# Kernel tuning notes

Measured on AMD Instinct MI355X. Metric: run time of the kernel, lower is better.

Reference implementation:

```python
import jax, jax.numpy as jnp
import numpy as np

DIM_HEAD = 128
HEADS = 16
SCALE = DIM_HEAD ** -0.5


def rotate_half(t):
    # '... (j d) -> ... j d' with j=2: split into first/second halves
    x1, x2 = jnp.split(t, 2, axis=-1)
    return jnp.concatenate((-x2, x1), axis=-1)


def apply_rope(pos, t):
    # pos: [n, d]; t: [..., n, d]
    return t * jnp.cos(pos) + rotate_half(t) * jnp.sin(pos)


def setup_inputs() -> dict:
    key = jax.random.key(0)
    k0, k1, k2, k3 = jax.random.split(key, 4)
    b, n, dim = 2, 2048, 2048
    inner = HEADS * DIM_HEAD
    return {
        "x": jax.random.normal(k0, (b, n, dim), jnp.float32),
        "Wq": jax.random.normal(k1, (dim, inner), jnp.float32) * 0.02,
        "Wkv": jax.random.normal(k2, (dim, 2 * DIM_HEAD), jnp.float32) * 0.02,
        "Wout": jax.random.normal(k3, (inner, dim), jnp.float32) * 0.02,
    }


def reference(x, Wq, Wkv, Wout):
    b, n, dim = x.shape
    # projections from the UN-normalized x (norm in original is dead code)
    q = x @ Wq                               # [b, n, h*d]
    kv = x @ Wkv                             # [b, n, 2d]
    k, v = jnp.split(kv, 2, axis=-1)         # each [b, n, d] (multi-query)
    q = q.reshape(b, n, HEADS, DIM_HEAD).transpose(0, 2, 1, 3)  # [b,h,n,d]

    # rotary positions
    inv_freq = 1.0 / (10000.0 ** (jnp.arange(0, DIM_HEAD, 2, dtype=jnp.float32) / DIM_HEAD))
    freqs = jnp.arange(n, dtype=jnp.float32)[:, None] * inv_freq[None, :]
    pos = jnp.concatenate((freqs, freqs), axis=-1)  # [n, d]

    q = apply_rope(pos, q) * SCALE
    k = apply_rope(pos, k)

    sim = jnp.einsum('bhid,bjd->bhij', q, k)  # [b,h,n,n]
    causal_mask = jnp.triu(jnp.ones((n, n), dtype=bool), 1)
    neg = -jnp.finfo(sim.dtype).max
    sim = jnp.where(causal_mask, neg, sim)
    sim = sim - jax.lax.stop_gradient(jnp.max(sim, axis=-1, keepdims=True))
    attn = jax.nn.softmax(sim, axis=-1)

    out = jnp.einsum('bhij,bjd->bhid', attn, v)          # [b,h,n,d]
    out = out.transpose(0, 2, 1, 3).reshape(b, n, HEADS * DIM_HEAD)
    return out @ Wout
```

## Files before the change

kernel.cpp:

```cpp
#include <hip/hip_runtime.h>
#include <hip/hip_bf16.h>
#include <cstddef>
#include <cstdint>

#define BATCH 2
#define SEQ   2048
#define DIM   2048
#define HEADS 16
#define DHEAD 128
#define INNER (HEADS * DHEAD)
#define MROWS (BATCH * SEQ)
#define ATT_SCALE 0.08838834764831845f
#define QK_SCALE (0.08838834764831845f * 1.4426950408889634f)
#define NEG_LOG2_10000_DIV64 (-13.287712379549449f / 64.0f)
#define M_HAT 12.0f

typedef __attribute__((ext_vector_type(8))) short short8;
typedef __attribute__((ext_vector_type(4))) short short4v;
typedef __attribute__((ext_vector_type(4))) float f32x4;

static __device__ __forceinline__ short f2bf(float x) {
    uint32_t u = __float_as_uint(x);
    uint32_t r = (u + 0x7fffu + ((u >> 16) & 1u)) >> 16;
    return (short)r;
}
static __device__ __forceinline__ float bf2f(short s) {
    return __uint_as_float(((uint32_t)(uint16_t)s) << 16);
}
static __device__ __forceinline__ short2 f2bf2(float a, float b) {
    __hip_bfloat162 h = __float22bfloat162_rn(make_float2(a, b));
    return *reinterpret_cast<short2*>(&h);
}

static __device__ __forceinline__ void glds16(const short* g, short* l) {
    __builtin_amdgcn_global_load_lds(
        (const __attribute__((address_space(1))) unsigned int*)g,
        (__attribute__((address_space(3))) unsigned int*)l, 16, 0, 0);
}

static __device__ __forceinline__ int swz_row(int r) {
    return (r & 3) | ((r >> 1) & 4);
}

static __device__ __forceinline__ void tcast_body(const float* __restrict__ W,
                                                  short* __restrict__ Wt,
                                                  int R, int C, int bx, int by,
                                                  int tid, float (*tile)[65]) {
    const int c0 = bx * 64, r0 = by * 64;
#pragma unroll
    for (int t = 0; t < 16; ++t) {
        int idx = tid + t * 256;
        int row = idx >> 6, col = idx & 63;
        tile[row][col] = W[(size_t)(r0 + row) * C + c0 + col];
    }
    __syncthreads();
#pragma unroll
    for (int t = 0; t < 16; ++t) {
        int idx = tid + t * 256;
        int r = idx >> 6, c = idx & 63;
        Wt[(size_t)(c0 + r) * R + r0 + c] = f2bf(tile[c][r]);
    }
}

__global__ __launch_bounds__(256) void prep(const float* __restrict__ x,
                                            short* __restrict__ xb,
                                            const float* __restrict__ Wq,
                                            short* __restrict__ Wt,
                                            const float* __restrict__ Wkv,
                                            short* __restrict__ Wkvt,
                                            const float* __restrict__ Wout,
                                            short* __restrict__ WtO,
                                            float2* __restrict__ lut) {
    __shared__ float tile[64][65];
    const int bid = blockIdx.x;
    const int tid = threadIdx.x;
    if (bid < 8192) {
        int i = bid * 256 + tid;
        float4 v = ((const float4*)x)[i];
        short2 s01 = f2bf2(v.x, v.y), s23 = f2bf2(v.z, v.w);
        short4v s = {s01.x, s01.y, s23.x, s23.y};
        ((short4v*)xb)[i] = s;
    } else if (bid < 9216) {
        int t = bid - 8192;
        tcast_body(Wq, Wt, DIM, INNER, t & 31, t >> 5, tid, tile);
    } else if (bid < 9344) {
        int t = bid - 9216;
        tcast_body(Wkv, Wkvt, DIM, 256, t & 3, t >> 2, tid, tile);
    } else if (bid < 10368) {
        int t = bid - 9344;
        tcast_body(Wout, WtO, INNER, DIM, t & 31, t >> 5, tid, tile);
    } else {
        int t = (bid - 10368) * 256 + tid;
        int pos = t >> 6, j = t & 63;
        float ang = (float)pos * exp2f((float)j * NEG_LOG2_10000_DIV64);
        lut[t] = make_float2(cosf(ang), sinf(ang));
    }
}

__global__ __launch_bounds__(256) void gemm_qkv(const short* __restrict__ A,
                                                const short* __restrict__ Bt,
                                                short* __restrict__ qout,
                                                short* __restrict__ kvout) {
    __shared__ __align__(16) short sA[128 * 32];
    __shared__ __align__(16) short sB[128 * 32];
    const int K = DIM;

    const int tid = threadIdx.x;
    const int w = tid >> 6, lane = tid & 63;
    const int ln = lane & 15, qr = lane >> 4;
    const int bm = blockIdx.y * 128, bn = blockIdx.x * 128;
    const int wm = (w >> 1) * 64, wn = (w & 1) * 64;

    const f32x4 zero4 = {0.f, 0.f, 0.f, 0.f};
    f32x4 acc[4][4];
#pragma unroll
    for (int mt = 0; mt < 4; ++mt)
#pragma unroll
        for (int nt = 0; nt < 4; ++nt) acc[mt][nt] = zero4;

    const int srow = lane >> 2;
    const short* pA = A + (size_t)(bm + w * 32 + srow) * K + (lane & 3) * 8;
    const short* pB = Bt + (size_t)(bn + w * 32 + srow) * K + (lane & 3) * 8;
    short* lA = &sA[(w * 32) * 32];
    short* lB = &sB[(w * 32) * 32];

    for (int k0 = 0; k0 < K; k0 += 32) {
        __syncthreads();
        glds16(pA + k0, lA);
        glds16(pA + k0 + (size_t)16 * K, lA + 512);
        glds16(pB + k0, lB);
        glds16(pB + k0 + (size_t)16 * K, lB + 512);
        __syncthreads();

        short8 af[4], bfr[4];
#pragma unroll
        for (int mt = 0; mt < 4; ++mt)
            af[mt] = *(const short8*)&sA[(wm + mt * 16 + ln) * 32 + qr * 8];
#pragma unroll
        for (int nt = 0; nt < 4; ++nt)
            bfr[nt] = *(const short8*)&sB[(wn + nt * 16 + ln) * 32 + qr * 8];
#pragma unroll
        for (int mt = 0; mt < 4; ++mt)
#pragma unroll
            for (int nt = 0; nt < 4; ++nt)
                acc[mt][nt] = __builtin_amdgcn_mfma_f32_16x16x32_bf16(
                    af[mt], bfr[nt], acc[mt][nt], 0, 0, 0);
    }

    short* C;
    int stride, colb;
    if (bn < INNER) { C = qout; stride = INNER; colb = bn; }
    else            { C = kvout; stride = 256;  colb = bn - INNER; }
#pragma unroll
    for (int mt = 0; mt < 4; ++mt)
#pragma unroll
        for (int nt = 0; nt < 4; ++nt)
#pragma unroll
            for (int r = 0; r < 4; ++r)
                C[(size_t)(bm + wm + mt * 16 + qr * 4 + r) * stride +
                  colb + wn + nt * 16 + ln] = f2bf(acc[mt][nt][r]);
}

__global__ __launch_bounds__(256) void gemm_bt(const short* __restrict__ A,
                                               const short* __restrict__ Bt,
                                               float* __restrict__ C,
                                               int M, int N, int K) {
    __shared__ __align__(16) short sA[128 * 32];
    __shared__ __align__(16) short sB[128 * 32];

    const int tid = threadIdx.x;
    const int w = tid >> 6, lane = tid & 63;
    const int ln = lane & 15, qr = lane >> 4;
    const int bm = blockIdx.y * 128, bn = blockIdx.x * 128;
    const int wm = (w >> 1) * 64, wn = (w & 1) * 64;

    const f32x4 zero4 = {0.f, 0.f, 0.f, 0.f};
    f32x4 acc[4][4];
#pragma unroll
    for (int mt = 0; mt < 4; ++mt)
#pragma unroll
        for (int nt = 0; nt < 4; ++nt) acc[mt][nt] = zero4;

    const int srow = lane >> 2;
    const short* pA = A + (size_t)(bm + w * 32 + srow) * K + (lane & 3) * 8;
    const short* pB = Bt + (size_t)(bn + w * 32 + srow) * K + (lane & 3) * 8;
    short* lA = &sA[(w * 32) * 32];
    short* lB = &sB[(w * 32) * 32];

    for (int k0 = 0; k0 < K; k0 += 32) {
        __syncthreads();
        glds16(pA + k0, lA);
        glds16(pA + k0 + (size_t)16 * K, lA + 512);
        glds16(pB + k0, lB);
        glds16(pB + k0 + (size_t)16 * K, lB + 512);
        __syncthreads();

        short8 af[4], bfr[4];
#pragma unroll
        for (int mt = 0; mt < 4; ++mt)
            af[mt] = *(const short8*)&sA[(wm + mt * 16 + ln) * 32 + qr * 8];
#pragma unroll
        for (int nt = 0; nt < 4; ++nt)
            bfr[nt] = *(const short8*)&sB[(wn + nt * 16 + ln) * 32 + qr * 8];
#pragma unroll
        for (int mt = 0; mt < 4; ++mt)
#pragma unroll
            for (int nt = 0; nt < 4; ++nt)
                acc[mt][nt] = __builtin_amdgcn_mfma_f32_16x16x32_bf16(
                    af[mt], bfr[nt], acc[mt][nt], 0, 0, 0);
    }

#pragma unroll
    for (int mt = 0; mt < 4; ++mt)
#pragma unroll
        for (int nt = 0; nt < 4; ++nt)
#pragma unroll
            for (int r = 0; r < 4; ++r)
                C[(size_t)(bm + wm + mt * 16 + qr * 4 + r) * N +
                  bn + wn + nt * 16 + ln] = acc[mt][nt][r];
}

__global__ __launch_bounds__(256) void rope_q_v(short* __restrict__ qb,
                                                const float2* __restrict__ lut) {
    int idx = blockIdx.x * 256 + threadIdx.x;
    int c = idx & 7;
    int rh = idx >> 3;
    int pos = (rh >> 4) & (SEQ - 1);
    short* row = qb + ((size_t)rh << 7);
    short8 a8 = *(short8*)&row[c * 8];
    short8 b8 = *(short8*)&row[64 + c * 8];
    const float2* lp = &lut[pos * 64 + c * 8];
    short8 o1, o2;
#pragma unroll
    for (int e = 0; e < 8; e += 2) {
        float2 cs0 = lp[e], cs1 = lp[e + 1];
        float a0 = bf2f(a8[e]), b0 = bf2f(b8[e]);
        float a1 = bf2f(a8[e + 1]), b1 = bf2f(b8[e + 1]);
        short2 p1 = f2bf2((a0 * cs0.x - b0 * cs0.y) * QK_SCALE,
                          (a1 * cs1.x - b1 * cs1.y) * QK_SCALE);
        short2 p2 = f2bf2((b0 * cs0.x + a0 * cs0.y) * QK_SCALE,
                          (b1 * cs1.x + a1 * cs1.y) * QK_SCALE);
        o1[e] = p1.x; o1[e + 1] = p1.y;
        o2[e] = p2.x; o2[e + 1] = p2.y;
    }
    *(short8*)&row[c * 8] = o1;
    *(short8*)&row[64 + c * 8] = o2;
}

__global__ __launch_bounds__(256) void prep_kv(const short* __restrict__ kvbb,
                                               short* __restrict__ kb,
                                               short* __restrict__ vt,
                                               const float2* __restrict__ lut) {
    __shared__ float tile[64][65];
    const int bid = blockIdx.x;
    const int tid = threadIdx.x;
    if (bid < 128) {
        const int b = bid >> 6;
        const int tile_id = bid & 63;
        const int p0 = (tile_id >> 1) * 64;
        const int d0 = (tile_id & 1) * 64;
#pragma unroll
        for (int t = 0; t < 16; ++t) {
            int idx = tid + t * 256;
            int row = idx >> 6, col = idx & 63;
            tile[row][col] = bf2f(kvbb[((size_t)(b * SEQ) + p0 + row) * 256 + 128 + d0 + col]);
        }
        __syncthreads();
#pragma unroll
        for (int t = 0; t < 16; ++t) {
            int idx = tid + t * 256;
            int r = idx >> 6, c = idx & 63;
            vt[((size_t)(b * DHEAD) + d0 + r) * SEQ + p0 + c] = f2bf(tile[c][r]);
        }
    } else {
        int t = (bid - 128) * 256 + tid;
        int c = t & 7;
        int bn = t >> 3;
        int pos = bn & (SEQ - 1);
        const short* row = kvbb + (size_t)bn * 256;
        short* orow = kb + ((size_t)bn << 7);
        short8 a8 = *(const short8*)&row[c * 8];
        short8 b8 = *(const short8*)&row[64 + c * 8];
        const float2* lp = &lut[pos * 64 + c * 8];
        short8 o1, o2;
#pragma unroll
        for (int e = 0; e < 8; e += 2) {
            float2 cs0 = lp[e], cs1 = lp[e + 1];
            float a0 = bf2f(a8[e]), b0 = bf2f(b8[e]);
            float a1 = bf2f(a8[e + 1]), b1 = bf2f(b8[e + 1]);
            short2 p1 = f2bf2(a0 * cs0.x - b0 * cs0.y, a1 * cs1.x - b1 * cs1.y);
            short2 p2 = f2bf2(b0 * cs0.x + a0 * cs0.y, b1 * cs1.x + a1 * cs1.y);
            o1[e] = p1.x; o1[e + 1] = p1.y;
            o2[e] = p2.x; o2[e + 1] = p2.y;
        }
        *(short8*)&orow[c * 8] = o1;
        *(short8*)&orow[64 + c * 8] = o2;
    }
}

__global__ __launch_bounds__(512) void attn_mfma(const short* __restrict__ qb,
                                                 const short* __restrict__ kb,
                                                 const short* __restrict__ vt,
                                                 short* __restrict__ o) {
    __shared__ __align__(16) short sK[2][2][64 * 128];
    __shared__ __align__(16) short sV[2][2][128 * 64];
    __shared__ float lred[4][2][64];

    const int bid = blockIdx.x;
    const int p = bid & 7;
    const int bh = bid >> 3;
    const int h = bh & (HEADS - 1);
    const int b = bh >> 4;

    const int tid = threadIdx.x;
    const int w = tid >> 6;
    const int g = w >> 2;
    const int wg = w & 3;
    const int lane = tid & 63;
    const int ln = lane & 15;
    const int qr = lane >> 4;

    const short* kbase = kb + (size_t)b * SEQ * DHEAD;
    const short* vbase = vt + (size_t)b * DHEAD * SEQ;

    int offK[4], offV[4], ldsK[4], ldsV[4];
#pragma unroll
    for (int t = 0; t < 4; ++t) {
        int rk = wg * 16 + t * 4 + (lane >> 4);
        int ck = (lane & 15) ^ swz_row(rk);
        offK[t] = rk * DHEAD + ck * 8;
        ldsK[t] = (wg * 16 + t * 4) * 128;
        int rv = wg * 32 + t * 8 + (lane >> 3);
        int cv = (lane & 7) ^ swz_row(rv);
        offV[t] = rv * SEQ + cv * 8;
        ldsV[t] = (wg * 32 + t * 8) * 64;
    }

    for (int ph = 0; ph < 2; ++ph) {
        const int it = ph ? p : (15 - p);
        const int i0 = it * 128;
        const int njt = 2 * it + 2;
        const int half = njt >> 1;
        const int igmax = i0 + wg * 32 + 31;

        short8 qf[2][4];
#pragma unroll
        for (int qs = 0; qs < 2; ++qs) {
            const size_t qrow =
                ((size_t)(b * SEQ + i0 + wg * 32 + qs * 16 + ln)) * INNER + h * DHEAD;
#pragma unroll
            for (int ks = 0; ks < 4; ++ks)
                qf[qs][ks] = *(const short8*)&qb[qrow + ks * 32 + qr * 8];
        }

        const f32x4 zero4 = {0.f, 0.f, 0.f, 0.f};
        const f32x4 mhat4 = {-M_HAT, -M_HAT, -M_HAT, -M_HAT};
        f32x4 oa[2][8];
#pragma unroll
        for (int qs = 0; qs < 2; ++qs)
#pragma unroll
            for (int dt = 0; dt < 8; ++dt) oa[qs][dt] = zero4;
        float lsum[2] = {0.f, 0.f};

        __syncthreads();
        {
            const size_t kof = (size_t)g * 64 * DHEAD;
            const size_t vof = (size_t)g * 64;
#pragma unroll
            for (int t = 0; t < 4; ++t)
                glds16(kbase + kof + offK[t], &sK[g][0][ldsK[t]]);
#pragma unroll
            for (int t = 0; t < 4; ++t)
                glds16(vbase + vof + offV[t], &sV[g][0][ldsV[t]]);
        }

        for (int k = 0; k < half; ++k) {
            const int cur = k & 1;
            const int jt = 2 * k + g;
            __syncthreads();
            if (k + 1 < half) {
                const size_t kof = (size_t)(jt + 2) * 64 * DHEAD;
                const size_t vof = (size_t)(jt + 2) * 64;
#pragma unroll
                for (int t = 0; t < 4; ++t)
                    glds16(kbase + kof + offK[t], &sK[g][cur ^ 1][ldsK[t]]);
#pragma unroll
                for (int t = 0; t < 4; ++t)
                    glds16(vbase + vof + offV[t], &sV[g][cur ^ 1][ldsV[t]]);
            }
            if (jt * 64 > igmax) continue;

            f32x4 sacc[2][4];
#pragma unroll
            for (int qs = 0; qs < 2; ++qs)
#pragma unroll
                for (int nt = 0; nt < 4; ++nt) sacc[qs][nt] = mhat4;
            __builtin_amdgcn_s_setprio(1);
#pragma unroll
            for (int nt = 0; nt < 4; ++nt) {
                const int row = ((nt >> 1) << 5) + ((ln >> 2) << 3) +
                                ((nt & 1) << 2) + (ln & 3);
                const int sw = ln & 7;
#pragma unroll
                for (int ks = 0; ks < 4; ++ks) {
                    short8 kf = *(const short8*)&sK[g][cur][row * 128 + ((4 * ks + qr) ^ sw) * 8];
                    sacc[0][nt] = __builtin_amdgcn_mfma_f32_16x16x32_bf16(
                        kf, qf[0][ks], sacc[0][nt], 0, 0, 0);
                    sacc[1][nt] = __builtin_amdgcn_mfma_f32_16x16x32_bf16(
                        kf, qf[1][ks], sacc[1][nt], 0, 0, 0);
                }
            }
            __builtin_amdgcn_s_setprio(0);

            short8 pb[2][2];
#pragma unroll
            for (int qs = 0; qs < 2; ++qs) {
                const int ig = i0 + wg * 32 + qs * 16 + ln;
                if (jt * 64 + 63 > ig) {
#pragma unroll
                    for (int nt = 0; nt < 4; ++nt)
#pragma unroll
                        for (int r = 0; r < 4; ++r) {
                            int jg = jt * 64 + ((nt >> 1) << 5) + qr * 8 +
                                     ((nt & 1) << 2) + r;
                            if (jg > ig) sacc[qs][nt][r] = -3.0e38f;
                        }
                }
                float rs = 0.f;
                float pv[4][4];
#pragma unroll
                for (int nt = 0; nt < 4; ++nt)
#pragma unroll
                    for (int r = 0; r < 4; ++r) {
                        float e = exp2f(sacc[qs][nt][r]);
                        pv[nt][r] = e;
                        rs += e;
                    }
                rs += __shfl_xor(rs, 16);
                rs += __shfl_xor(rs, 32);
                lsum[qs] += rs;
#pragma unroll
                for (int kb2 = 0; kb2 < 2; ++kb2) {
                    short2* pp = (short2*)&pb[qs][kb2];
                    pp[0] = f2bf2(pv[2 * kb2][0], pv[2 * kb2][1]);
                    pp[1] = f2bf2(pv[2 * kb2][2], pv[2 * kb2][3]);
                    pp[2] = f2bf2(pv[2 * kb2 + 1][0], pv[2 * kb2 + 1][1]);
                    pp[3] = f2bf2(pv[2 * kb2 + 1][2], pv[2 * kb2 + 1][3]);
                }
            }

            __builtin_amdgcn_s_setprio(1);
#pragma unroll
            for (int kb2 = 0; kb2 < 2; ++kb2) {
#pragma unroll
                for (int dt = 0; dt < 8; ++dt) {
                    const int row = dt * 16 + ln;
                    short8 vf = *(const short8*)&sV[g][cur][row * 64 +
                        ((4 * kb2 + qr) ^ swz_row(row)) * 8];
                    oa[0][dt] = __builtin_amdgcn_mfma_f32_16x16x32_bf16(
                        vf, pb[0][kb2], oa[0][dt], 0, 0, 0);
                    oa[1][dt] = __builtin_amdgcn_mfma_f32_16x16x32_bf16(
                        vf, pb[1][kb2], oa[1][dt], 0, 0, 0);
                }
            }
            __builtin_amdgcn_s_setprio(0);
        }

        f32x4* cb = (f32x4*)&sK[1][0][0];
        __syncthreads();
        if (g == 1) {
#pragma unroll
            for (int dt = 0; dt < 8; ++dt)
                cb[dt * 256 + wg * 64 + lane] = oa[0][dt];
            lred[wg][0][lane] = lsum[0];
            lred[wg][1][lane] = lsum[1];
        }
        __syncthreads();
        if (g == 0) {
#pragma unroll
            for (int dt = 0; dt < 8; ++dt)
                oa[0][dt] += cb[dt * 256 + wg * 64 + lane];
            lsum[0] += lred[wg][0][lane];
            lsum[1] += lred[wg][1][lane];
        }
        __syncthreads();
        if (g == 1) {
#pragma unroll
            for (int dt = 0; dt < 8; ++dt)
                cb[dt * 256 + wg * 64 + lane] = oa[1][dt];
        }
        __syncthreads();
        if (g == 0) {
#pragma unroll
            for (int dt = 0; dt < 8; ++dt)
                oa[1][dt] += cb[dt * 256 + wg * 64 + lane];
#pragma unroll
            for (int qs = 0; qs < 2; ++qs) {
                const float invl = 1.f / lsum[qs];
                short* orow = o + ((size_t)(b * SEQ + i0 + wg * 32 + qs * 16 + ln)) * INNER +
                              h * DHEAD;
#pragma unroll
                for (int dt = 0; dt < 8; ++dt) {
                    short2 s01 = f2bf2(oa[qs][dt][0] * invl, oa[qs][dt][1] * invl);
                    short2 s23 = f2bf2(oa[qs][dt][2] * invl, oa[qs][dt][3] * invl);
                    short4v sv = {s01.x, s01.y, s23.x, s23.y};
                    *(short4v*)&orow[dt * 16 + qr * 4] = sv;
                }
            }
        }
    }
}

extern "C" void kernel_launch(void* const* d_in, const int* in_sizes, int n_in,
                              void* d_out, int out_size, void* d_ws, size_t ws_size,
                              hipStream_t stream) {
    const float* x    = (const float*)d_in[0];
    const float* Wq   = (const float*)d_in[1];
    const float* Wkv  = (const float*)d_in[2];
    const float* Wout = (const float*)d_in[3];
    float* out = (float*)d_out;

    short* xb    = (short*)d_ws;
    short* Wt    = xb + (size_t)MROWS * DIM;
    short* Wkvt  = Wt + (size_t)DIM * INNER;
    short* WtO   = Wkvt + (size_t)256 * DIM;
    short* qb    = WtO + (size_t)DIM * INNER;
    short* kvbb  = qb + (size_t)MROWS * INNER;
    short* kb    = kvbb + (size_t)MROWS * 256;
    short* vt    = kb + (size_t)MROWS * DHEAD;
    float2* lut  = (float2*)(vt + (size_t)BATCH * DHEAD * SEQ);
    short* ob    = xb;

    prep<<<10880, 256, 0, stream>>>(x, xb, Wq, Wt, Wkv, Wkvt, Wout, WtO, lut);
    gemm_qkv<<<dim3(18, 32), 256, 0, stream>>>(xb, Wt, qb, kvbb);
    rope_q_v<<<(MROWS * HEADS * 8) / 256, 256, 0, stream>>>(qb, lut);
    prep_kv<<<256, 256, 0, stream>>>(kvbb, kb, vt, lut);
    attn_mfma<<<256, 512, 0, stream>>>(qb, kb, vt, ob);
    gemm_bt<<<dim3(DIM / 128, MROWS / 128), 256, 0, stream>>>(ob, WtO, out, MROWS, DIM, INNER);
}
```

Measured before the change: 290.7 us.

## Fuse RoPE into QKV GEMM epilogue, remap GEMM blocks per XCD, vectorize transposes

RoPE for Q (with the softmax scale) and for K is now applied in the QKV GEMM epilogue. Each block stages its accumulator tile in LDS so it can read the partner half-dimension. This removes the separate rope_q_v kernel and the K-rope half of prep_kv, along with their extra global read/write passes. Both GEMMs also remap block IDs round-robin across the 8 XCDs for better L2 locality, and the weight transpose-cast uses float4 loads and short4 stores. The cost is a larger LDS footprint and an extra sync in the QKV epilogue, plus more scattered per-element stores there.

```diff
diff --git a/kernel.cpp b/kernel.cpp
--- a/kernel.cpp
+++ b/kernel.cpp
@@ -48,17 +48,24 @@
                                                   int tid, float (*tile)[65]) {
     const int c0 = bx * 64, r0 = by * 64;
 #pragma unroll
-    for (int t = 0; t < 16; ++t) {
+    for (int t = 0; t < 4; ++t) {
         int idx = tid + t * 256;
-        int row = idx >> 6, col = idx & 63;
-        tile[row][col] = W[(size_t)(r0 + row) * C + c0 + col];
+        int row = idx >> 4, col4 = idx & 15;
+        float4 v = *(const float4*)&W[(size_t)(r0 + row) * C + c0 + col4 * 4];
+        tile[row][col4 * 4 + 0] = v.x;
+        tile[row][col4 * 4 + 1] = v.y;
+        tile[row][col4 * 4 + 2] = v.z;
+        tile[row][col4 * 4 + 3] = v.w;
     }
     __syncthreads();
 #pragma unroll
-    for (int t = 0; t < 16; ++t) {
+    for (int t = 0; t < 4; ++t) {
         int idx = tid + t * 256;
-        int r = idx >> 6, c = idx & 63;
-        Wt[(size_t)(c0 + r) * R + r0 + c] = f2bf(tile[c][r]);
+        int r = idx >> 4, c4 = idx & 15;
+        short2 s01 = f2bf2(tile[c4 * 4 + 0][r], tile[c4 * 4 + 1][r]);
+        short2 s23 = f2bf2(tile[c4 * 4 + 2][r], tile[c4 * 4 + 3][r]);
+        short4v s = {s01.x, s01.y, s23.x, s23.y};
+        *(short4v*)&Wt[(size_t)(c0 + r) * R + r0 + c4 * 4] = s;
     }
 }
 
@@ -100,15 +107,21 @@
 __global__ __launch_bounds__(256) void gemm_qkv(const short* __restrict__ A,
                                                 const short* __restrict__ Bt,
                                                 short* __restrict__ qout,
-                                                short* __restrict__ kvout) {
-    __shared__ __align__(16) short sA[128 * 32];
-    __shared__ __align__(16) short sB[128 * 32];
+                                                short* __restrict__ kvout,
+                                                short* __restrict__ kbout,
+                                                const float2* __restrict__ lut) {
+    __shared__ __align__(16) char smem[128 * 132 * 4];
+    short* sA = (short*)smem;
+    short* sB = (short*)(smem + 8192);
+    float* tx = (float*)smem;
     const int K = DIM;
 
     const int tid = threadIdx.x;
     const int w = tid >> 6, lane = tid & 63;
     const int ln = lane & 15, qr = lane >> 4;
-    const int bm = blockIdx.y * 128, bn = blockIdx.x * 128;
+    const int flat = blockIdx.y * gridDim.x + blockIdx.x;
+    const int wg = (flat & 7) * 72 + (flat >> 3);
+    const int bm = (wg / 18) * 128, bn = (wg % 18) * 128;
     const int wm = (w >> 1) * 64, wn = (w & 1) * 64;
 
     const f32x4 zero4 = {0.f, 0.f, 0.f, 0.f};
@@ -147,18 +160,50 @@
                     af[mt], bfr[nt], acc[mt][nt], 0, 0, 0);
     }
 
-    short* C;
-    int stride, colb;
-    if (bn < INNER) { C = qout; stride = INNER; colb = bn; }
-    else            { C = kvout; stride = 256;  colb = bn - INNER; }
-#pragma unroll
-    for (int mt = 0; mt < 4; ++mt)
-#pragma unroll
-        for (int nt = 0; nt < 4; ++nt)
-#pragma unroll
-            for (int r = 0; r < 4; ++r)
-                C[(size_t)(bm + wm + mt * 16 + qr * 4 + r) * stride +
-                  colb + wn + nt * 16 + ln] = f2bf(acc[mt][nt][r]);
+    if (bn <= INNER) {
+        const float scale = (bn < INNER) ? QK_SCALE : 1.0f;
+        __syncthreads();
+#pragma unroll
+        for (int mt = 0; mt < 4; ++mt)
+#pragma unroll
+            for (int nt = 0; nt < 4; ++nt)
+#pragma unroll
+                for (int r = 0; r < 4; ++r)
+                    tx[(wm + mt * 16 + qr * 4 + r) * 132 + wn + nt * 16 + ln] =
+                        acc[mt][nt][r];
+        __syncthreads();
+#pragma unroll
+        for (int mt = 0; mt < 4; ++mt) {
+#pragma unroll
+            for (int nt = 0; nt < 4; ++nt) {
+#pragma unroll
+                for (int r = 0; r < 4; ++r) {
+                    const int row_r = wm + mt * 16 + qr * 4 + r;
+                    const int cn = wn + nt * 16 + ln;
+                    const int pos = (bm + row_r) & (SEQ - 1);
+                    const float own = acc[mt][nt][r];
+                    const float partner = tx[row_r * 132 + (cn ^ 64)];
+                    const float2 cs = lut[pos * 64 + (cn & 63)];
+                    const float out = (wn == 0)
+                                          ? (own * cs.x - partner * cs.y) * scale
+                                          : (own * cs.x + partner * cs.y) * scale;
+                    if (bn < INNER)
+                        qout[(size_t)(bm + row_r) * INNER + bn + cn] = f2bf(out);
+                    else
+                        kbout[(size_t)(bm + row_r) * DHEAD + cn] = f2bf(out);
+                }
+            }
+        }
+    } else {
+#pragma unroll
+        for (int mt = 0; mt < 4; ++mt)
+#pragma unroll
+            for (int nt = 0; nt < 4; ++nt)
+#pragma unroll
+                for (int r = 0; r < 4; ++r)
+                    kvout[(size_t)(bm + wm + mt * 16 + qr * 4 + r) * 256 + 128 +
+                          wn + nt * 16 + ln] = f2bf(acc[mt][nt][r]);
+    }
 }
 
 __global__ __launch_bounds__(256) void gemm_bt(const short* __restrict__ A,
@@ -171,7 +216,9 @@
     const int tid = threadIdx.x;
     const int w = tid >> 6, lane = tid & 63;
     const int ln = lane & 15, qr = lane >> 4;
-    const int bm = blockIdx.y * 128, bn = blockIdx.x * 128;
+    const int flat = blockIdx.y * gridDim.x + blockIdx.x;
+    const int wg = (flat & 7) * 64 + (flat >> 3);
+    const int bm = (wg >> 4) * 128, bn = (wg & 15) * 128;
     const int wm = (w >> 1) * 64, wn = (w & 1) * 64;
 
     const f32x4 zero4 = {0.f, 0.f, 0.f, 0.f};
@@ -220,81 +267,27 @@
                   bn + wn + nt * 16 + ln] = acc[mt][nt][r];
 }
 
-__global__ __launch_bounds__(256) void rope_q_v(short* __restrict__ qb,
-                                                const float2* __restrict__ lut) {
-    int idx = blockIdx.x * 256 + threadIdx.x;
-    int c = idx & 7;
-    int rh = idx >> 3;
-    int pos = (rh >> 4) & (SEQ - 1);
-    short* row = qb + ((size_t)rh << 7);
-    short8 a8 = *(short8*)&row[c * 8];
-    short8 b8 = *(short8*)&row[64 + c * 8];
-    const float2* lp = &lut[pos * 64 + c * 8];
-    short8 o1, o2;
-#pragma unroll
-    for (int e = 0; e < 8; e += 2) {
-        float2 cs0 = lp[e], cs1 = lp[e + 1];
-        float a0 = bf2f(a8[e]), b0 = bf2f(b8[e]);
-        float a1 = bf2f(a8[e + 1]), b1 = bf2f(b8[e + 1]);
-        short2 p1 = f2bf2((a0 * cs0.x - b0 * cs0.y) * QK_SCALE,
-                          (a1 * cs1.x - b1 * cs1.y) * QK_SCALE);
-        short2 p2 = f2bf2((b0 * cs0.x + a0 * cs0.y) * QK_SCALE,
-                          (b1 * cs1.x + a1 * cs1.y) * QK_SCALE);
-        o1[e] = p1.x; o1[e + 1] = p1.y;
-        o2[e] = p2.x; o2[e + 1] = p2.y;
-    }
-    *(short8*)&row[c * 8] = o1;
-    *(short8*)&row[64 + c * 8] = o2;
-}
-
 __global__ __launch_bounds__(256) void prep_kv(const short* __restrict__ kvbb,
-                                               short* __restrict__ kb,
-                                               short* __restrict__ vt,
-                                               const float2* __restrict__ lut) {
+                                               short* __restrict__ vt) {
     __shared__ float tile[64][65];
     const int bid = blockIdx.x;
     const int tid = threadIdx.x;
-    if (bid < 128) {
-        const int b = bid >> 6;
-        const int tile_id = bid & 63;
-        const int p0 = (tile_id >> 1) * 64;
-        const int d0 = (tile_id & 1) * 64;
-#pragma unroll
-        for (int t = 0; t < 16; ++t) {
-            int idx = tid + t * 256;
-            int row = idx >> 6, col = idx & 63;
-            tile[row][col] = bf2f(kvbb[((size_t)(b * SEQ) + p0 + row) * 256 + 128 + d0 + col]);
-        }
-        __syncthreads();
-#pragma unroll
-        for (int t = 0; t < 16; ++t) {
-            int idx = tid + t * 256;
-            int r = idx >> 6, c = idx & 63;
-            vt[((size_t)(b * DHEAD) + d0 + r) * SEQ + p0 + c] = f2bf(tile[c][r]);
-        }
-    } else {
-        int t = (bid - 128) * 256 + tid;
-        int c = t & 7;
-        int bn = t >> 3;
-        int pos = bn & (SEQ - 1);
-        const short* row = kvbb + (size_t)bn * 256;
-        short* orow = kb + ((size_t)bn << 7);
-        short8 a8 = *(const short8*)&row[c * 8];
-        short8 b8 = *(const short8*)&row[64 + c * 8];
-        const float2* lp = &lut[pos * 64 + c * 8];
-        short8 o1, o2;
-#pragma unroll
-        for (int e = 0; e < 8; e += 2) {
-            float2 cs0 = lp[e], cs1 = lp[e + 1];
-            float a0 = bf2f(a8[e]), b0 = bf2f(b8[e]);
-            float a1 = bf2f(a8[e + 1]), b1 = bf2f(b8[e + 1]);
-            short2 p1 = f2bf2(a0 * cs0.x - b0 * cs0.y, a1 * cs1.x - b1 * cs1.y);
-            short2 p2 = f2bf2(b0 * cs0.x + a0 * cs0.y, b1 * cs1.x + a1 * cs1.y);
-            o1[e] = p1.x; o1[e + 1] = p1.y;
-            o2[e] = p2.x; o2[e + 1] = p2.y;
-        }
-        *(short8*)&orow[c * 8] = o1;
-        *(short8*)&orow[64 + c * 8] = o2;
+    const int b = bid >> 6;
+    const int tile_id = bid & 63;
+    const int p0 = (tile_id >> 1) * 64;
+    const int d0 = (tile_id & 1) * 64;
+#pragma unroll
+    for (int t = 0; t < 16; ++t) {
+        int idx = tid + t * 256;
+        int row = idx >> 6, col = idx & 63;
+        tile[row][col] = bf2f(kvbb[((size_t)(b * SEQ) + p0 + row) * 256 + 128 + d0 + col]);
+    }
+    __syncthreads();
+#pragma unroll
+    for (int t = 0; t < 16; ++t) {
+        int idx = tid + t * 256;
+        int r = idx >> 6, c = idx & 63;
+        vt[((size_t)(b * DHEAD) + d0 + r) * SEQ + p0 + c] = f2bf(tile[c][r]);
     }
 }
 
@@ -532,9 +525,8 @@
     short* ob    = xb;
 
     prep<<<10880, 256, 0, stream>>>(x, xb, Wq, Wt, Wkv, Wkvt, Wout, WtO, lut);
-    gemm_qkv<<<dim3(18, 32), 256, 0, stream>>>(xb, Wt, qb, kvbb);
-    rope_q_v<<<(MROWS * HEADS * 8) / 256, 256, 0, stream>>>(qb, lut);
-    prep_kv<<<256, 256, 0, stream>>>(kvbb, kb, vt, lut);
+    gemm_qkv<<<dim3(18, 32), 256, 0, stream>>>(xb, Wt, qb, kvbb, kb, lut);
+    prep_kv<<<128, 256, 0, stream>>>(kvbb, vt);
     attn_mfma<<<256, 512, 0, stream>>>(qb, kb, vt, ob);
-    gemm_bt<<<dim3(DIM / 128, MROWS / 128), 256, 0, stream>>>(ob, WtO, out, MROWS, DIM, INNER);
-}
+    gemm_bt<<<dim3(16, 32), 256, 0, stream>>>(ob, WtO, out, MROWS, DIM, INNER);
+}
```

Measured after the change: 323.4 us. 1.11x slower.
